# Optimization experiments

Hardware: AMD Instinct MI355X
Metric: run time of the kernel (lower is better)

## Reference

```python
import jax, jax.numpy as jnp
import numpy as np

V, E, H, A, L = 32000, 512, 1024, 1024, 2
B, T, S = 16, 64, 64


def gru_cell(x, h, W_ih, W_hh, b_ih, b_hh):
    # torch GRUCell math: gates ordered (r, z, n)
    gx = x @ W_ih.T + b_ih
    gh = h @ W_hh.T + b_hh
    xr, xz, xn = jnp.split(gx, 3, axis=-1)
    hr, hz, hn = jnp.split(gh, 3, axis=-1)
    r = jax.nn.sigmoid(xr + hr)
    z = jax.nn.sigmoid(xz + hz)
    n = jnp.tanh(xn + r * hn)
    return (1.0 - z) * n + z * h


def setup_inputs() -> dict:
    key = jax.random.key(0)
    ks = jax.random.split(key, 20)
    s = 0.02
    return {
        "tgt": jax.random.randint(ks[0], (B, T), 0, V),
        "hidden": jax.random.normal(ks[1], (L, B, H), jnp.float32) * 0.1,
        "encoder_outputs": jax.random.normal(ks[2], (B, S, H), jnp.float32),
        "emb": jax.random.normal(ks[3], (V, E), jnp.float32) * s,
        "Wq": jax.random.normal(ks[4], (H, A), jnp.float32) * s,
        "Wk": jax.random.normal(ks[5], (H, A), jnp.float32) * s,
        "v_att": jax.random.normal(ks[6], (A,), jnp.float32) * s,
        "W_ih0": jax.random.normal(ks[7], (3 * H, E + H), jnp.float32) * s,
        "W_hh0": jax.random.normal(ks[8], (3 * H, H), jnp.float32) * s,
        "b_ih0": jnp.zeros((3 * H,), jnp.float32),
        "b_hh0": jnp.zeros((3 * H,), jnp.float32),
        "W_ih1": jax.random.normal(ks[9], (3 * H, H), jnp.float32) * s,
        "W_hh1": jax.random.normal(ks[10], (3 * H, H), jnp.float32) * s,
        "b_ih1": jnp.zeros((3 * H,), jnp.float32),
        "b_hh1": jnp.zeros((3 * H,), jnp.float32),
        "W_out": jax.random.normal(ks[11], (V, H), jnp.float32) * s,
        "b_out": jnp.zeros((V,), jnp.float32),
    }


def reference(tgt, hidden, encoder_outputs, emb, Wq, Wk, v_att,
              W_ih0, W_hh0, b_ih0, b_hh0, W_ih1, W_hh1, b_ih1, b_hh1,
              W_out, b_out):
    # Teacher forcing (ratio=1.0), dropout in eval mode (identity).
    keys_proj = jnp.einsum('bsh,ha->bsa', encoder_outputs, Wk)  # precompute W_k K
    emb_tok = emb[tgt]  # [B,T,E]

    def step(carry, x_t):
        h0, h1 = carry  # each [B,H]
        # Bahdanau attention: query = last-layer hidden
        q = jnp.einsum('bh,ha->ba', h1, Wq)
        scores = jnp.einsum('bsa,a->bs', jnp.tanh(q[:, None, :] + keys_proj), v_att)
        attn = jax.nn.softmax(scores, axis=-1)
        ctx = jnp.einsum('bs,bsh->bh', attn, encoder_outputs)
        rnn_in = jnp.concatenate([x_t, ctx], axis=-1)  # [B, E+H]
        h0n = gru_cell(rnn_in, h0, W_ih0, W_hh0, b_ih0, b_hh0)
        h1n = gru_cell(h0n, h1, W_ih1, W_hh1, b_ih1, b_hh1)
        logits = h1n @ W_out.T + b_out  # [B,V]
        return (h0n, h1n), logits

    (_, _), logits = jax.lax.scan(step, (hidden[0], hidden[1]),
                                  jnp.swapaxes(emb_tok, 0, 1))  # xs: [T,B,E]
    return jnp.swapaxes(logits, 0, 1)  # [B,T,V]
```

## Files before the change

kernel.cpp:

```cpp
#include <hip/hip_runtime.h>
#include <hip/hip_bf16.h>
#include <math.h>

typedef __bf16 bf16x8 __attribute__((ext_vector_type(8)));
typedef float  f32x4  __attribute__((ext_vector_type(4)));

__device__ __forceinline__ float sigm(float x){ return 1.0f/(1.0f+expf(-x)); }
__device__ __forceinline__ f32x4 ld4(const float* p){ return *(const f32x4*)p; }
__device__ __forceinline__ void split2(float x, __bf16* h, __bf16* l){
  __bf16 hh = (__bf16)x; *h = hh; *l = (__bf16)(x - (float)hh);
}

__global__ __launch_bounds__(256) void k_transpose(const float* __restrict__ in,
                                                   float* __restrict__ out, int R, int C){
  __shared__ float tile[32][33];
  int c0 = blockIdx.x*32, r0 = blockIdx.y*32;
  int tx = threadIdx.x & 31, ty = threadIdx.x >> 5;
  for(int i=ty;i<32;i+=8) tile[i][tx] = in[(size_t)(r0+i)*C + c0+tx];
  __syncthreads();
  for(int i=ty;i<32;i+=8) out[(size_t)(c0+i)*R + r0+tx] = tile[tx][i];
}

__global__ __launch_bounds__(256) void k_gather(const int* __restrict__ tgt,
                                                const float* __restrict__ emb,
                                                float* __restrict__ emb_tok){
  int m = blockIdx.x;
  int t = m >> 4, b = m & 15;
  int row = tgt[b*64 + t];
  const float* src = emb + (size_t)row*512;
  float* dst = emb_tok + (size_t)m*512;
  for(int e=threadIdx.x;e<512;e+=256) dst[e] = src[e];
}

__global__ __launch_bounds__(256) void k_gemm_s(
    const float* __restrict__ A, int lda,
    const float* __restrict__ Bt, int ldb,
    const float* __restrict__ bias,
    float* __restrict__ C, int N, int K)
{
  __shared__ __align__(16) __bf16 Ash[128][40];
  __shared__ __align__(16) __bf16 Asl[128][40];
  __shared__ __align__(16) __bf16 Bsh[64][40];
  __shared__ __align__(16) __bf16 Bsl[64][40];
  int tid = threadIdx.x;
  int m0 = blockIdx.x*128, n0 = blockIdx.y*64;
  int lane = tid & 63, wave = tid >> 6;
  int wr = wave >> 1, wc = wave & 1;
  int qq = lane >> 4, rr = lane & 15;
  f32x4 acc[4][2] = {};
  int ar = tid >> 1, ak = (tid & 1)*16;
  int br = tid >> 2, bk = (tid & 3)*8;
  for(int k0=0;k0<K;k0+=32){
    const float* ap = A + (size_t)(m0+ar)*lda + k0 + ak;
    f32x4 a0 = ld4(ap), a1 = ld4(ap+4), a2 = ld4(ap+8), a3 = ld4(ap+12);
    const float* bp = Bt + (size_t)(n0+br)*ldb + k0 + bk;
    f32x4 b0 = ld4(bp), b1 = ld4(bp+4);
    __syncthreads();
    #pragma unroll
    for(int e=0;e<4;++e){
      split2(a0[e], &Ash[ar][ak+e],    &Asl[ar][ak+e]);
      split2(a1[e], &Ash[ar][ak+4+e],  &Asl[ar][ak+4+e]);
      split2(a2[e], &Ash[ar][ak+8+e],  &Asl[ar][ak+8+e]);
      split2(a3[e], &Ash[ar][ak+12+e], &Asl[ar][ak+12+e]);
      split2(b0[e], &Bsh[br][bk+e],    &Bsl[br][bk+e]);
      split2(b1[e], &Bsh[br][bk+4+e],  &Bsl[br][bk+4+e]);
    }
    __syncthreads();
    bf16x8 afh[4], afl[4], bfh[2], bfl[2];
    #pragma unroll
    for(int mi=0;mi<4;++mi){
      afh[mi] = *(const bf16x8*)&Ash[wr*64 + mi*16 + rr][qq*8];
      afl[mi] = *(const bf16x8*)&Asl[wr*64 + mi*16 + rr][qq*8];
    }
    #pragma unroll
    for(int ni=0;ni<2;++ni){
      bfh[ni] = *(const bf16x8*)&Bsh[wc*32 + ni*16 + rr][qq*8];
      bfl[ni] = *(const bf16x8*)&Bsl[wc*32 + ni*16 + rr][qq*8];
    }
    #pragma unroll
    for(int mi=0;mi<4;++mi)
      #pragma unroll
      for(int ni=0;ni<2;++ni){
        acc[mi][ni] = __builtin_amdgcn_mfma_f32_16x16x32_bf16(afh[mi], bfh[ni], acc[mi][ni], 0,0,0);
        acc[mi][ni] = __builtin_amdgcn_mfma_f32_16x16x32_bf16(afl[mi], bfh[ni], acc[mi][ni], 0,0,0);
        acc[mi][ni] = __builtin_amdgcn_mfma_f32_16x16x32_bf16(afh[mi], bfl[ni], acc[mi][ni], 0,0,0);
      }
  }
  #pragma unroll
  for(int mi=0;mi<4;++mi)
    #pragma unroll
    for(int ni=0;ni<2;++ni)
      #pragma unroll
      for(int i=0;i<4;++i){
        int m = m0 + wr*64 + mi*16 + qq*4 + i;
        int n = n0 + wc*32 + ni*16 + rr;
        C[(size_t)m*N + n] = acc[mi][ni][i] + (bias? bias[n] : 0.f);
      }
}

__global__ __launch_bounds__(256) void k_pack_w(const float* __restrict__ W,
                                                __bf16* __restrict__ Wp){
  int jt = blockIdx.x, tid = threadIdx.x;
  #pragma unroll
  for(int it=0; it<8; ++it){
    int pos = it*256 + tid;
    int kt = pos>>6, l = pos&63;
    const float* src = W + (size_t)(jt*16 + (l&15))*1024 + kt*32 + (l>>4)*8;
    f32x4 s0 = ld4(src), s1 = ld4(src+4);
    bf16x8 vh, vl;
    #pragma unroll
    for(int e=0;e<4;++e){
      __bf16 h, lo;
      split2(s0[e], &h, &lo); vh[e]   = h; vl[e]   = lo;
      split2(s1[e], &h, &lo); vh[4+e] = h; vl[4+e] = lo;
    }
    __bf16* dst = Wp + ((size_t)(jt*32 + kt))*1024 + l*8;
    *(bf16x8*)dst       = vh;
    *(bf16x8*)(dst+512) = vl;
  }
}

__global__ __launch_bounds__(256) void k_split_h(const float* __restrict__ hidden,
    __bf16* __restrict__ h0h, __bf16* __restrict__ h0l,
    __bf16* __restrict__ h1h, __bf16* __restrict__ h1l){
  int i = blockIdx.x*256 + threadIdx.x;
  float x = hidden[i];
  if(i < 16384) split2(x, &h0h[i], &h0l[i]);
  else { int j = i - 16384; split2(x, &h1h[j], &h1l[j]); }
}

__device__ __forceinline__ void mfma_gemv16(const __bf16* __restrict__ hh,
                                            const __bf16* __restrict__ hl,
                                            const __bf16* __restrict__ Wp, int jt,
                                            float* __restrict__ out, int ldo,
                                            f32x4* red){
  int tid = threadIdx.x, lane = tid & 63, w = tid >> 6;
  const __bf16* Ah = hh + (lane&15)*1024 + (lane>>4)*8;
  const __bf16* Al = hl + (lane&15)*1024 + (lane>>4)*8;
  const __bf16* Bp = Wp + ((size_t)jt*32 + w*8)*1024 + lane*8;
  f32x4 acc = {0.f,0.f,0.f,0.f};
  #pragma unroll
  for(int kk=0;kk<8;++kk){
    int k0 = (w*8 + kk)*32;
    bf16x8 ah = *(const bf16x8*)(Ah + k0);
    bf16x8 al = *(const bf16x8*)(Al + k0);
    bf16x8 bh = *(const bf16x8*)(Bp + kk*1024);
    bf16x8 bl = *(const bf16x8*)(Bp + kk*1024 + 512);
    acc = __builtin_amdgcn_mfma_f32_16x16x32_bf16(ah, bh, acc, 0,0,0);
    acc = __builtin_amdgcn_mfma_f32_16x16x32_bf16(al, bh, acc, 0,0,0);
    acc = __builtin_amdgcn_mfma_f32_16x16x32_bf16(ah, bl, acc, 0,0,0);
  }
  red[w*64 + lane] = acc;
  __syncthreads();
  if(tid < 64){
    f32x4 s = red[tid] + red[64+tid] + red[128+tid] + red[192+tid];
    int j = jt*16 + (tid & 15);
    #pragma unroll
    for(int i=0;i<4;++i) out[(size_t)((tid>>4)*4 + i)*ldo + j] = s[i];
  }
}

__global__ __launch_bounds__(256) void k_boot(const __bf16* __restrict__ hh,
                                              const __bf16* __restrict__ hl,
                                              const __bf16* __restrict__ Wp,
                                              float* __restrict__ gh0){
  __shared__ f32x4 red[256];
  mfma_gemv16(hh, hl, Wp, blockIdx.x, gh0, 3072, red);
}

__global__ __launch_bounds__(256) void k_step1(const __bf16* __restrict__ h1h,
                                               const __bf16* __restrict__ h1l,
                                               const __bf16* __restrict__ Whh1p,
                                               const __bf16* __restrict__ Wqp,
                                               float* __restrict__ gh1,
                                               float* __restrict__ q){
  __shared__ f32x4 red[256];
  int blk = blockIdx.x;
  if(blk < 192) mfma_gemv16(h1h, h1l, Whh1p, blk,     gh1, 3072, red);
  else          mfma_gemv16(h1h, h1l, Wqp,   blk-192, q,   1024, red);
}

__global__ __launch_bounds__(512) void k_step2(const float* __restrict__ q,
                                               const float* __restrict__ kp,
                                               const float* __restrict__ v_att,
                                               float* __restrict__ escore){
  int pair = blockIdx.x*8 + (threadIdx.x >> 6);
  int b = pair >> 6;
  int lane = threadIdx.x & 63;
  const float* qp  = q  + b*1024 + lane*16;
  const float* kpp = kp + (size_t)pair*1024 + lane*16;
  const float* vp  = v_att + lane*16;
  float acc = 0.f;
  #pragma unroll
  for(int i=0;i<4;++i){
    f32x4 qv = ld4(qp+i*4), kv = ld4(kpp+i*4), vv = ld4(vp+i*4);
    #pragma unroll
    for(int e=0;e<4;++e) acc += vv[e]*tanhf(qv[e]+kv[e]);
  }
  #pragma unroll
  for(int o=1;o<64;o<<=1) acc += __shfl_xor(acc, o);
  if(lane==0) escore[pair] = expf(acc);
}

__global__ __launch_bounds__(512) void k_step3(int t,
    const float* __restrict__ escore, const float* __restrict__ EW,
    const float* __restrict__ GX0x, const float* __restrict__ gh0,
    const float* __restrict__ b_hh0,
    const float* __restrict__ h0_in, float* __restrict__ h0_out,
    __bf16* __restrict__ h0h, __bf16* __restrict__ h0l)
{
  __shared__ float part[8][4][16][3];
  __shared__ float dred[4][16];
  __shared__ float sden[4];
  int blk = blockIdx.x, tid = threadIdx.x;
  int jt = blk >> 2, bq = blk & 3;
  int lane = tid & 63, w = tid >> 6;
  int bl = lane >> 4, jl = lane & 15;
  int b = bq*4 + bl;
  int col = jt*16 + jl;
  float a0=0.f, a1=0.f, a2=0.f;
  const float* ep  = escore + b*64 + w*8;
  const float* ewp = EW + ((size_t)(b*64 + w*8))*3072 + col;
  #pragma unroll
  for(int si=0; si<8; ++si){
    float e = ep[si];
    const float* r = ewp + (size_t)si*3072;
    a0 += e*r[0]; a1 += e*r[1024]; a2 += e*r[2048];
  }
  part[w][bl][jl][0]=a0; part[w][bl][jl][1]=a1; part[w][bl][jl][2]=a2;
  if(tid < 64){
    int bb = tid >> 4, si = tid & 15;
    const float* e2 = escore + (bq*4 + bb)*64;
    dred[bb][si] = e2[si] + e2[si+16] + e2[si+32] + e2[si+48];
  }
  __syncthreads();
  if(tid < 4){
    float d = 0.f;
    #pragma unroll
    for(int i=0;i<16;++i) d += dred[tid][i];
    sden[tid] = d;
  }
  __syncthreads();
  if(tid < 64){
    float xr=0.f, xz=0.f, xn=0.f;
    #pragma unroll
    for(int k=0;k<8;++k){ xr+=part[k][bl][jl][0]; xz+=part[k][bl][jl][1]; xn+=part[k][bl][jl][2]; }
    float inv = 1.0f / sden[bl];
    int j = col;
    const float* gx = GX0x + ((size_t)t*16 + b)*3072 + j;
    const float* g0 = gh0 + (size_t)b*3072 + j;
    float r = sigm(xr*inv + gx[0]    + g0[0]    + b_hh0[j]);
    float z = sigm(xz*inv + gx[1024] + g0[1024] + b_hh0[1024+j]);
    float n = tanhf(xn*inv + gx[2048] + r*(g0[2048] + b_hh0[2048+j]));
    float hnew = (1.f-z)*n + z*h0_in[b*1024 + j];
    h0_out[b*1024 + j] = hnew;
    split2(hnew, &h0h[b*1024 + j], &h0l[b*1024 + j]);
  }
}

__global__ __launch_bounds__(256) void k_step4(int t,
    const __bf16* __restrict__ h0h, const __bf16* __restrict__ h0l,
    const __bf16* __restrict__ Wih1p, const __bf16* __restrict__ Whh0p,
    const float* __restrict__ b_ih1, const float* __restrict__ b_hh1,
    const float* __restrict__ gh1,
    const float* __restrict__ h1_in, float* __restrict__ h1_out,
    __bf16* __restrict__ h1h, __bf16* __restrict__ h1l,
    __bf16* __restrict__ Hb, float* __restrict__ gh0)
{
  __shared__ f32x4 red[256];
  __shared__ float xg[3][16][16];
  int blk = blockIdx.x, tid = threadIdx.x;
  if(blk >= 64){
    mfma_gemv16(h0h, h0l, Whh0p, blk-64, gh0, 3072, red);
    return;
  }
  int lane = tid & 63, w = tid >> 6;
  const __bf16* Ah = h0h + (lane&15)*1024 + (lane>>4)*8;
  const __bf16* Al = h0l + (lane&15)*1024 + (lane>>4)*8;
  #pragma unroll
  for(int g=0; g<3; ++g){
    int jt = g*64 + blk;
    const __bf16* Bp = Wih1p + ((size_t)jt*32 + w*8)*1024 + lane*8;
    f32x4 acc = {0.f,0.f,0.f,0.f};
    #pragma unroll
    for(int kk=0;kk<8;++kk){
      int k0 = (w*8 + kk)*32;
      bf16x8 ah = *(const bf16x8*)(Ah + k0);
      bf16x8 al = *(const bf16x8*)(Al + k0);
      bf16x8 bh = *(const bf16x8*)(Bp + kk*1024);
      bf16x8 bl = *(const bf16x8*)(Bp + kk*1024 + 512);
      acc = __builtin_amdgcn_mfma_f32_16x16x32_bf16(ah, bh, acc, 0,0,0);
      acc = __builtin_amdgcn_mfma_f32_16x16x32_bf16(al, bh, acc, 0,0,0);
      acc = __builtin_amdgcn_mfma_f32_16x16x32_bf16(ah, bl, acc, 0,0,0);
    }
    if(g) __syncthreads();
    red[w*64 + lane] = acc;
    __syncthreads();
    if(tid < 64){
      f32x4 s = red[tid] + red[64+tid] + red[128+tid] + red[192+tid];
      #pragma unroll
      for(int i=0;i<4;++i) xg[g][(tid>>4)*4 + i][tid&15] = s[i];
    }
  }
  __syncthreads();
  int b = tid >> 4, jl = tid & 15, j = blk*16 + jl;
  float xr = xg[0][b][jl] + b_ih1[j];
  float xz = xg[1][b][jl] + b_ih1[1024+j];
  float xn = xg[2][b][jl] + b_ih1[2048+j];
  const float* g1 = gh1 + (size_t)b*3072 + j;
  float r = sigm(xr + g1[0]    + b_hh1[j]);
  float z = sigm(xz + g1[1024] + b_hh1[1024+j]);
  float n = tanhf(xn + r*(g1[2048] + b_hh1[2048+j]));
  float hnew = (1.f-z)*n + z*h1_in[b*1024 + j];
  h1_out[b*1024 + j] = hnew;
  split2(hnew, &h1h[b*1024 + j], &h1l[b*1024 + j]);
  Hb[((size_t)t*16 + b)*1024 + j] = (__bf16)hnew;
}

__global__ __launch_bounds__(512) void k_logits(
    const __bf16* __restrict__ Hb, const float* __restrict__ Wout,
    const float* __restrict__ b_out, float* __restrict__ out)
{
  int c = blockIdx.x & 7, j = blockIdx.x >> 3;
  int x = j & 3, y = (j >> 2)*8 + c;
  if(y >= 250) return;
  int tm0 = x*256, tn0 = y*128;
  __shared__ __align__(16) __bf16 As[256][40];
  __shared__ __align__(16) __bf16 Bs[128][40];
  int tid = threadIdx.x;
  int lane = tid & 63, wave = tid >> 6;
  int wr = wave >> 1, wc = wave & 1;
  int qq = lane >> 4, rr = lane & 15;
  f32x4 acc[4][4] = {};
  int ar = tid >> 2, ak = (tid & 3) * 8;
  for(int k0=0;k0<1024;k0+=32){
    bf16x8 a0v = *(const bf16x8*)(Hb + (size_t)(tm0+ar)*1024     + k0 + ak);
    bf16x8 a1v = *(const bf16x8*)(Hb + (size_t)(tm0+ar+128)*1024 + k0 + ak);
    const float* bp = Wout + (size_t)(tn0+ar)*1024 + k0 + ak;
    f32x4 f0 = ld4(bp), f1 = ld4(bp+4);
    __syncthreads();
    *(bf16x8*)&As[ar][ak]     = a0v;
    *(bf16x8*)&As[ar+128][ak] = a1v;
    bf16x8 bv;
    #pragma unroll
    for(int i=0;i<4;++i){ bv[i]=(__bf16)f0[i]; bv[4+i]=(__bf16)f1[i]; }
    *(bf16x8*)&Bs[ar][ak] = bv;
    __syncthreads();
    bf16x8 af[4], bfr[4];
    #pragma unroll
    for(int mi=0;mi<4;++mi) af[mi]  = *(const bf16x8*)&As[wr*64 + mi*16 + rr][qq*8];
    #pragma unroll
    for(int ni=0;ni<4;++ni) bfr[ni] = *(const bf16x8*)&Bs[wc*64 + ni*16 + rr][qq*8];
    #pragma unroll
    for(int mi=0;mi<4;++mi)
      #pragma unroll
      for(int ni=0;ni<4;++ni)
        acc[mi][ni] = __builtin_amdgcn_mfma_f32_16x16x32_bf16(af[mi], bfr[ni], acc[mi][ni], 0,0,0);
  }
  #pragma unroll
  for(int mi=0;mi<4;++mi)
    #pragma unroll
    for(int ni=0;ni<4;++ni)
      #pragma unroll
      for(int i=0;i<4;++i){
        int m = tm0 + wr*64 + mi*16 + qq*4 + i;
        int v = tn0 + wc*64 + ni*16 + rr;
        int bb = m & 15, tt = m >> 4;
        out[((size_t)bb*64 + tt)*32000 + v] = acc[mi][ni][i] + b_out[v];
      }
}

extern "C" void kernel_launch(void* const* d_in, const int* in_sizes, int n_in,
                              void* d_out, int out_size, void* d_ws, size_t ws_size,
                              hipStream_t stream){
  const int*   tgt    = (const int*)d_in[0];
  const float* hidden = (const float*)d_in[1];
  const float* enc    = (const float*)d_in[2];
  const float* emb    = (const float*)d_in[3];
  const float* Wq     = (const float*)d_in[4];
  const float* Wk     = (const float*)d_in[5];
  const float* v_att  = (const float*)d_in[6];
  const float* W_ih0  = (const float*)d_in[7];
  const float* W_hh0  = (const float*)d_in[8];
  const float* b_ih0  = (const float*)d_in[9];
  const float* b_hh0  = (const float*)d_in[10];
  const float* W_ih1  = (const float*)d_in[11];
  const float* W_hh1  = (const float*)d_in[12];
  const float* b_ih1  = (const float*)d_in[13];
  const float* b_hh1  = (const float*)d_in[14];
  const float* W_out  = (const float*)d_in[15];
  const float* b_out  = (const float*)d_in[16];
  float* out = (float*)d_out;

  float* ws = (float*)d_ws;
  size_t off = 0;
  auto alloc = [&](size_t n){ float* p = ws + off; off += n; return p; };
  float*  kp     = alloc((size_t)1024*1024);
  float*  GX0x   = alloc((size_t)1024*3072);
  float*  EW     = alloc((size_t)1024*3072);
  __bf16* Whh0p  = (__bf16*)alloc((size_t)3072*1024);
  __bf16* Whh1p  = (__bf16*)alloc((size_t)3072*1024);
  __bf16* Wih1p  = (__bf16*)alloc((size_t)3072*1024);
  __bf16* Wqp    = (__bf16*)alloc((size_t)1024*1024);
  float*  gh0    = alloc((size_t)16*3072);
  float*  gh1    = alloc((size_t)16*3072);
  float*  q      = alloc((size_t)16*1024);
  float*  escore = alloc((size_t)16*64);
  float*  h0A    = alloc((size_t)16*1024);
  float*  h0B    = alloc((size_t)16*1024);
  float*  h1A    = alloc((size_t)16*1024);
  float*  h1B    = alloc((size_t)16*1024);
  __bf16* h0sh   = (__bf16*)alloc((size_t)8192);
  __bf16* h0sl   = (__bf16*)alloc((size_t)8192);
  __bf16* h1sh   = (__bf16*)alloc((size_t)8192);
  __bf16* h1sl   = (__bf16*)alloc((size_t)8192);
  __bf16* Hb     = (__bf16*)alloc((size_t)512*1024);
  float*  REGION = alloc((size_t)1572864);
  float*  emb_tok = REGION;
  float*  WT      = REGION + 524288;
  (void)ws_size; (void)in_sizes; (void)n_in; (void)out_size;

  k_gather<<<1024,256,0,stream>>>(tgt, emb, emb_tok);
  k_transpose<<<dim3(32,32),256,0,stream>>>(Wk, WT, 1024, 1024);
  k_gemm_s<<<dim3(8,16),256,0,stream>>>(enc,1024, WT,1024, nullptr, kp, 1024, 1024);
  k_gemm_s<<<dim3(8,48),256,0,stream>>>(emb_tok,512, W_ih0,1536, b_ih0, GX0x, 3072, 512);
  k_gemm_s<<<dim3(8,48),256,0,stream>>>(enc,1024, W_ih0+512,1536, nullptr, EW, 3072, 1024);
  k_transpose<<<dim3(32,32),256,0,stream>>>(Wq, WT, 1024, 1024);
  k_pack_w<<<64,256,0,stream>>>(WT, Wqp);
  k_pack_w<<<192,256,0,stream>>>(W_hh0, Whh0p);
  k_pack_w<<<192,256,0,stream>>>(W_hh1, Whh1p);
  k_pack_w<<<192,256,0,stream>>>(W_ih1, Wih1p);
  k_split_h<<<128,256,0,stream>>>(hidden, h0sh, h0sl, h1sh, h1sl);
  k_boot<<<192,256,0,stream>>>(h0sh, h0sl, Whh0p, gh0);

  for(int t=0;t<64;++t){
    const float* h0i = (t==0)? hidden            : ((t&1)? h0A : h0B);
    float*       h0o = (t&1)? h0B : h0A;
    const float* h1i = (t==0)? hidden + 16*1024  : ((t&1)? h1A : h1B);
    float*       h1o = (t&1)? h1B : h1A;
    k_step1<<<256,256,0,stream>>>(h1sh, h1sl, Whh1p, Wqp, gh1, q);
    k_step2<<<128,512,0,stream>>>(q, kp, v_att, escore);
    k_step3<<<256,512,0,stream>>>(t, escore, EW, GX0x, gh0, b_hh0, h0i, h0o, h0sh, h0sl);
    k_step4<<<256,256,0,stream>>>(t, h0sh, h0sl, Wih1p, Whh0p, b_ih1, b_hh1, gh1,
                                  h1i, h1o, h1sh, h1sl, Hb, gh0);
  }

  k_logits<<<1024,512,0,stream>>>(Hb, W_out, b_out, out);
}
```

Before: 2.093 ms.

## Fuse attention scoring into query GEMV kernel and pre-convert W_out to bf16

Combines the Wq projection with partial attention score computation per 16-wide slice, moving softmax reduction into the GRU0 update kernel, so each timestep uses three launches instead of four. GEMV blocks are widened to 8 waves with shorter K loops per wave. Wq is packed directly from its original layout instead of via a transpose, and W_out is converted to bf16 once before the logits GEMM to halve its reads there. This adds an extra conversion pass and workspace aliasing that must not overlap live data.

Result: slower. 2.166 ms (+3.5%).

```diff
diff --git a/kernel.cpp b/kernel.cpp
--- a/kernel.cpp
+++ b/kernel.cpp
@@ -4,6 +4,8 @@
 
 typedef __bf16 bf16x8 __attribute__((ext_vector_type(8)));
 typedef float  f32x4  __attribute__((ext_vector_type(4)));
+
+#define MFMA16 __builtin_amdgcn_mfma_f32_16x16x32_bf16
 
 __device__ __forceinline__ float sigm(float x){ return 1.0f/(1.0f+expf(-x)); }
 __device__ __forceinline__ f32x4 ld4(const float* p){ return *(const f32x4*)p; }
@@ -81,9 +83,9 @@
     for(int mi=0;mi<4;++mi)
       #pragma unroll
       for(int ni=0;ni<2;++ni){
-        acc[mi][ni] = __builtin_amdgcn_mfma_f32_16x16x32_bf16(afh[mi], bfh[ni], acc[mi][ni], 0,0,0);
-        acc[mi][ni] = __builtin_amdgcn_mfma_f32_16x16x32_bf16(afl[mi], bfh[ni], acc[mi][ni], 0,0,0);
-        acc[mi][ni] = __builtin_amdgcn_mfma_f32_16x16x32_bf16(afh[mi], bfl[ni], acc[mi][ni], 0,0,0);
+        acc[mi][ni] = MFMA16(afh[mi], bfh[ni], acc[mi][ni], 0,0,0);
+        acc[mi][ni] = MFMA16(afl[mi], bfh[ni], acc[mi][ni], 0,0,0);
+        acc[mi][ni] = MFMA16(afh[mi], bfl[ni], acc[mi][ni], 0,0,0);
       }
   }
   #pragma unroll
@@ -120,6 +122,28 @@
   }
 }
 
+__global__ __launch_bounds__(256) void k_pack_wT(const float* __restrict__ W, int ldw,
+                                                 __bf16* __restrict__ Wp){
+  int jt = blockIdx.x, tid = threadIdx.x;
+  #pragma unroll
+  for(int it=0; it<8; ++it){
+    int pos = it*256 + tid;
+    int kt = pos>>6, l = pos&63;
+    int j = jt*16 + (l&15);
+    int kbase = kt*32 + (l>>4)*8;
+    bf16x8 vh, vl;
+    #pragma unroll
+    for(int e=0;e<8;++e){
+      float x = W[(size_t)(kbase+e)*ldw + j];
+      __bf16 h = (__bf16)x;
+      vh[e] = h; vl[e] = (__bf16)(x - (float)h);
+    }
+    __bf16* dst = Wp + ((size_t)(jt*32 + kt))*1024 + l*8;
+    *(bf16x8*)dst       = vh;
+    *(bf16x8*)(dst+512) = vl;
+  }
+}
+
 __global__ __launch_bounds__(256) void k_split_h(const float* __restrict__ hidden,
     __bf16* __restrict__ h0h, __bf16* __restrict__ h0l,
     __bf16* __restrict__ h1h, __bf16* __restrict__ h1l){
@@ -129,136 +153,181 @@
   else { int j = i - 16384; split2(x, &h1h[j], &h1l[j]); }
 }
 
-__device__ __forceinline__ void mfma_gemv16(const __bf16* __restrict__ hh,
-                                            const __bf16* __restrict__ hl,
-                                            const __bf16* __restrict__ Wp, int jt,
-                                            float* __restrict__ out, int ldo,
-                                            f32x4* red){
+__global__ __launch_bounds__(256) void k_cvt16(const float* __restrict__ in,
+                                               __bf16* __restrict__ out){
+  int i = blockIdx.x*256 + threadIdx.x;
+  const float* p = in + (size_t)i*8;
+  f32x4 f0 = ld4(p), f1 = ld4(p+4);
+  bf16x8 v;
+  #pragma unroll
+  for(int e=0;e<4;++e){ v[e] = (__bf16)f0[e]; v[4+e] = (__bf16)f1[e]; }
+  *(bf16x8*)(out + (size_t)i*8) = v;
+}
+
+__device__ __forceinline__ void gemv_w8(const __bf16* __restrict__ hh,
+                                        const __bf16* __restrict__ hl,
+                                        const __bf16* __restrict__ Wp, int jt,
+                                        float* __restrict__ out, int ldo,
+                                        f32x4* red){
   int tid = threadIdx.x, lane = tid & 63, w = tid >> 6;
   const __bf16* Ah = hh + (lane&15)*1024 + (lane>>4)*8;
   const __bf16* Al = hl + (lane&15)*1024 + (lane>>4)*8;
-  const __bf16* Bp = Wp + ((size_t)jt*32 + w*8)*1024 + lane*8;
+  const __bf16* Bp = Wp + ((size_t)jt*32 + w*4)*1024 + lane*8;
   f32x4 acc = {0.f,0.f,0.f,0.f};
   #pragma unroll
-  for(int kk=0;kk<8;++kk){
-    int k0 = (w*8 + kk)*32;
+  for(int kk=0;kk<4;++kk){
+    int k0 = (w*4 + kk)*32;
     bf16x8 ah = *(const bf16x8*)(Ah + k0);
     bf16x8 al = *(const bf16x8*)(Al + k0);
     bf16x8 bh = *(const bf16x8*)(Bp + kk*1024);
     bf16x8 bl = *(const bf16x8*)(Bp + kk*1024 + 512);
-    acc = __builtin_amdgcn_mfma_f32_16x16x32_bf16(ah, bh, acc, 0,0,0);
-    acc = __builtin_amdgcn_mfma_f32_16x16x32_bf16(al, bh, acc, 0,0,0);
-    acc = __builtin_amdgcn_mfma_f32_16x16x32_bf16(ah, bl, acc, 0,0,0);
+    acc = MFMA16(ah, bh, acc, 0,0,0);
+    acc = MFMA16(al, bh, acc, 0,0,0);
+    acc = MFMA16(ah, bl, acc, 0,0,0);
   }
   red[w*64 + lane] = acc;
   __syncthreads();
   if(tid < 64){
-    f32x4 s = red[tid] + red[64+tid] + red[128+tid] + red[192+tid];
+    f32x4 s = red[tid];
+    #pragma unroll
+    for(int k=1;k<8;++k) s += red[k*64 + tid];
     int j = jt*16 + (tid & 15);
     #pragma unroll
     for(int i=0;i<4;++i) out[(size_t)((tid>>4)*4 + i)*ldo + j] = s[i];
   }
 }
 
-__global__ __launch_bounds__(256) void k_boot(const __bf16* __restrict__ hh,
+__global__ __launch_bounds__(512) void k_boot(const __bf16* __restrict__ hh,
                                               const __bf16* __restrict__ hl,
                                               const __bf16* __restrict__ Wp,
                                               float* __restrict__ gh0){
-  __shared__ f32x4 red[256];
-  mfma_gemv16(hh, hl, Wp, blockIdx.x, gh0, 3072, red);
-}
-
-__global__ __launch_bounds__(256) void k_step1(const __bf16* __restrict__ h1h,
-                                               const __bf16* __restrict__ h1l,
-                                               const __bf16* __restrict__ Whh1p,
-                                               const __bf16* __restrict__ Wqp,
-                                               float* __restrict__ gh1,
-                                               float* __restrict__ q){
-  __shared__ f32x4 red[256];
-  int blk = blockIdx.x;
-  if(blk < 192) mfma_gemv16(h1h, h1l, Whh1p, blk,     gh1, 3072, red);
-  else          mfma_gemv16(h1h, h1l, Wqp,   blk-192, q,   1024, red);
-}
-
-__global__ __launch_bounds__(512) void k_step2(const float* __restrict__ q,
-                                               const float* __restrict__ kp,
-                                               const float* __restrict__ v_att,
-                                               float* __restrict__ escore){
-  int pair = blockIdx.x*8 + (threadIdx.x >> 6);
-  int b = pair >> 6;
-  int lane = threadIdx.x & 63;
-  const float* qp  = q  + b*1024 + lane*16;
-  const float* kpp = kp + (size_t)pair*1024 + lane*16;
-  const float* vp  = v_att + lane*16;
-  float acc = 0.f;
-  #pragma unroll
-  for(int i=0;i<4;++i){
-    f32x4 qv = ld4(qp+i*4), kv = ld4(kpp+i*4), vv = ld4(vp+i*4);
-    #pragma unroll
-    for(int e=0;e<4;++e) acc += vv[e]*tanhf(qv[e]+kv[e]);
-  }
-  #pragma unroll
-  for(int o=1;o<64;o<<=1) acc += __shfl_xor(acc, o);
-  if(lane==0) escore[pair] = expf(acc);
-}
-
-__global__ __launch_bounds__(512) void k_step3(int t,
-    const float* __restrict__ escore, const float* __restrict__ EW,
+  __shared__ f32x4 red[512];
+  gemv_w8(hh, hl, Wp, blockIdx.x, gh0, 3072, red);
+}
+
+__global__ __launch_bounds__(512) void k_SA(
+    const __bf16* __restrict__ h1h, const __bf16* __restrict__ h1l,
+    const __bf16* __restrict__ Whh1p, const __bf16* __restrict__ Wqp,
+    const float* __restrict__ kp, const float* __restrict__ v_att,
+    float* __restrict__ gh1, float* __restrict__ parts)
+{
+  __shared__ f32x4 red[512];
+  __shared__ float qs[16][16];
+  int blk = blockIdx.x, tid = threadIdx.x;
+  if(blk < 192){ gemv_w8(h1h, h1l, Whh1p, blk, gh1, 3072, red); return; }
+  int slice = blk - 192;
+  {
+    int lane = tid & 63, w = tid >> 6;
+    const __bf16* Ah = h1h + (lane&15)*1024 + (lane>>4)*8;
+    const __bf16* Al = h1l + (lane&15)*1024 + (lane>>4)*8;
+    const __bf16* Bp = Wqp + ((size_t)slice*32 + w*4)*1024 + lane*8;
+    f32x4 acc = {0.f,0.f,0.f,0.f};
+    #pragma unroll
+    for(int kk=0;kk<4;++kk){
+      int k0 = (w*4 + kk)*32;
+      bf16x8 ah = *(const bf16x8*)(Ah + k0);
+      bf16x8 al = *(const bf16x8*)(Al + k0);
+      bf16x8 bh = *(const bf16x8*)(Bp + kk*1024);
+      bf16x8 bl = *(const bf16x8*)(Bp + kk*1024 + 512);
+      acc = MFMA16(ah, bh, acc, 0,0,0);
+      acc = MFMA16(al, bh, acc, 0,0,0);
+      acc = MFMA16(ah, bl, acc, 0,0,0);
+    }
+    red[w*64 + lane] = acc;
+    __syncthreads();
+    if(tid < 64){
+      f32x4 s = red[tid];
+      #pragma unroll
+      for(int k=1;k<8;++k) s += red[k*64 + tid];
+      #pragma unroll
+      for(int i=0;i<4;++i) qs[(tid>>4)*4 + i][tid&15] = s[i];
+    }
+    __syncthreads();
+  }
+  const float* vp = v_att + slice*16;
+  f32x4 v0 = ld4(vp), v1 = ld4(vp+4), v2 = ld4(vp+8), v3 = ld4(vp+12);
+  #pragma unroll
+  for(int r=0;r<2;++r){
+    int pair = r*512 + tid;
+    int b = pair >> 6;
+    const float* kpr = kp + (size_t)pair*1024 + slice*16;
+    f32x4 c0 = ld4(kpr), c1 = ld4(kpr+4), c2 = ld4(kpr+8), c3 = ld4(kpr+12);
+    float acc = 0.f;
+    #pragma unroll
+    for(int e=0;e<4;++e){
+      acc += v0[e]*tanhf(qs[b][e]     + c0[e]);
+      acc += v1[e]*tanhf(qs[b][4+e]   + c1[e]);
+      acc += v2[e]*tanhf(qs[b][8+e]   + c2[e]);
+      acc += v3[e]*tanhf(qs[b][12+e]  + c3[e]);
+    }
+    parts[(size_t)slice*1024 + pair] = acc;
+  }
+}
+
+__global__ __launch_bounds__(512) void k_SB(int t,
+    const float* __restrict__ parts, const float* __restrict__ EW,
     const float* __restrict__ GX0x, const float* __restrict__ gh0,
     const float* __restrict__ b_hh0,
     const float* __restrict__ h0_in, float* __restrict__ h0_out,
     __bf16* __restrict__ h0h, __bf16* __restrict__ h0l)
 {
+  __shared__ float ssum[256][2];
+  __shared__ float sc[4][64];
+  __shared__ float sden[4];
   __shared__ float part[8][4][16][3];
-  __shared__ float dred[4][16];
-  __shared__ float sden[4];
   int blk = blockIdx.x, tid = threadIdx.x;
   int jt = blk >> 2, bq = blk & 3;
+  {
+    int p = tid >> 1, hf = tid & 1;
+    int pair = bq*256 + p;
+    const float* pp = parts + (size_t)(hf*32)*1024 + pair;
+    float s = 0.f;
+    #pragma unroll
+    for(int k=0;k<32;++k) s += pp[(size_t)k*1024];
+    ssum[p][hf] = s;
+  }
+  __syncthreads();
+  if(tid < 256) sc[tid>>6][tid&63] = expf(ssum[tid][0] + ssum[tid][1]);
+  __syncthreads();
+  if(tid < 4){
+    float d = 0.f;
+    #pragma unroll
+    for(int s2=0;s2<64;++s2) d += sc[tid][s2];
+    sden[tid] = d;
+  }
+  __syncthreads();
   int lane = tid & 63, w = tid >> 6;
   int bl = lane >> 4, jl = lane & 15;
-  int b = bq*4 + bl;
-  int col = jt*16 + jl;
+  int b = bq*4 + bl, col = jt*16 + jl;
   float a0=0.f, a1=0.f, a2=0.f;
-  const float* ep  = escore + b*64 + w*8;
   const float* ewp = EW + ((size_t)(b*64 + w*8))*3072 + col;
   #pragma unroll
   for(int si=0; si<8; ++si){
-    float e = ep[si];
-    const float* r = ewp + (size_t)si*3072;
-    a0 += e*r[0]; a1 += e*r[1024]; a2 += e*r[2048];
+    float e = sc[bl][w*8 + si];
+    const float* r2 = ewp + (size_t)si*3072;
+    a0 += e*r2[0]; a1 += e*r2[1024]; a2 += e*r2[2048];
   }
   part[w][bl][jl][0]=a0; part[w][bl][jl][1]=a1; part[w][bl][jl][2]=a2;
+  __syncthreads();
   if(tid < 64){
-    int bb = tid >> 4, si = tid & 15;
-    const float* e2 = escore + (bq*4 + bb)*64;
-    dred[bb][si] = e2[si] + e2[si+16] + e2[si+32] + e2[si+48];
-  }
-  __syncthreads();
-  if(tid < 4){
-    float d = 0.f;
-    #pragma unroll
-    for(int i=0;i<16;++i) d += dred[tid][i];
-    sden[tid] = d;
-  }
-  __syncthreads();
-  if(tid < 64){
+    int bl2 = tid >> 4, jl2 = tid & 15;
+    int b2 = bq*4 + bl2, j = jt*16 + jl2;
     float xr=0.f, xz=0.f, xn=0.f;
     #pragma unroll
-    for(int k=0;k<8;++k){ xr+=part[k][bl][jl][0]; xz+=part[k][bl][jl][1]; xn+=part[k][bl][jl][2]; }
-    float inv = 1.0f / sden[bl];
-    int j = col;
-    const float* gx = GX0x + ((size_t)t*16 + b)*3072 + j;
-    const float* g0 = gh0 + (size_t)b*3072 + j;
+    for(int k=0;k<8;++k){ xr+=part[k][bl2][jl2][0]; xz+=part[k][bl2][jl2][1]; xn+=part[k][bl2][jl2][2]; }
+    float inv = 1.0f / sden[bl2];
+    const float* gx = GX0x + ((size_t)t*16 + b2)*3072 + j;
+    const float* g0 = gh0 + (size_t)b2*3072 + j;
     float r = sigm(xr*inv + gx[0]    + g0[0]    + b_hh0[j]);
     float z = sigm(xz*inv + gx[1024] + g0[1024] + b_hh0[1024+j]);
     float n = tanhf(xn*inv + gx[2048] + r*(g0[2048] + b_hh0[2048+j]));
-    float hnew = (1.f-z)*n + z*h0_in[b*1024 + j];
-    h0_out[b*1024 + j] = hnew;
-    split2(hnew, &h0h[b*1024 + j], &h0l[b*1024 + j]);
-  }
-}
-
-__global__ __launch_bounds__(256) void k_step4(int t,
+    float hnew = (1.f-z)*n + z*h0_in[b2*1024 + j];
+    h0_out[b2*1024 + j] = hnew;
+    split2(hnew, &h0h[b2*1024 + j], &h0l[b2*1024 + j]);
+  }
+}
+
+__global__ __launch_bounds__(512) void k_SC(int t,
     const __bf16* __restrict__ h0h, const __bf16* __restrict__ h0l,
     const __bf16* __restrict__ Wih1p, const __bf16* __restrict__ Whh0p,
     const float* __restrict__ b_ih1, const float* __restrict__ b_hh1,
@@ -267,58 +336,58 @@
     __bf16* __restrict__ h1h, __bf16* __restrict__ h1l,
     __bf16* __restrict__ Hb, float* __restrict__ gh0)
 {
-  __shared__ f32x4 red[256];
+  __shared__ f32x4 red[1536];
   __shared__ float xg[3][16][16];
   int blk = blockIdx.x, tid = threadIdx.x;
-  if(blk >= 64){
-    mfma_gemv16(h0h, h0l, Whh0p, blk-64, gh0, 3072, red);
-    return;
-  }
+  if(blk >= 64){ gemv_w8(h0h, h0l, Whh0p, blk-64, gh0, 3072, red); return; }
   int lane = tid & 63, w = tid >> 6;
   const __bf16* Ah = h0h + (lane&15)*1024 + (lane>>4)*8;
   const __bf16* Al = h0l + (lane&15)*1024 + (lane>>4)*8;
   #pragma unroll
   for(int g=0; g<3; ++g){
-    int jt = g*64 + blk;
-    const __bf16* Bp = Wih1p + ((size_t)jt*32 + w*8)*1024 + lane*8;
+    const __bf16* Bp = Wih1p + ((size_t)(g*64 + blk)*32 + w*4)*1024 + lane*8;
     f32x4 acc = {0.f,0.f,0.f,0.f};
     #pragma unroll
-    for(int kk=0;kk<8;++kk){
-      int k0 = (w*8 + kk)*32;
+    for(int kk=0;kk<4;++kk){
+      int k0 = (w*4 + kk)*32;
       bf16x8 ah = *(const bf16x8*)(Ah + k0);
       bf16x8 al = *(const bf16x8*)(Al + k0);
       bf16x8 bh = *(const bf16x8*)(Bp + kk*1024);
       bf16x8 bl = *(const bf16x8*)(Bp + kk*1024 + 512);
-      acc = __builtin_amdgcn_mfma_f32_16x16x32_bf16(ah, bh, acc, 0,0,0);
-      acc = __builtin_amdgcn_mfma_f32_16x16x32_bf16(al, bh, acc, 0,0,0);
-      acc = __builtin_amdgcn_mfma_f32_16x16x32_bf16(ah, bl, acc, 0,0,0);
-    }
-    if(g) __syncthreads();
-    red[w*64 + lane] = acc;
-    __syncthreads();
-    if(tid < 64){
-      f32x4 s = red[tid] + red[64+tid] + red[128+tid] + red[192+tid];
-      #pragma unroll
-      for(int i=0;i<4;++i) xg[g][(tid>>4)*4 + i][tid&15] = s[i];
-    }
-  }
-  __syncthreads();
-  int b = tid >> 4, jl = tid & 15, j = blk*16 + jl;
-  float xr = xg[0][b][jl] + b_ih1[j];
-  float xz = xg[1][b][jl] + b_ih1[1024+j];
-  float xn = xg[2][b][jl] + b_ih1[2048+j];
-  const float* g1 = gh1 + (size_t)b*3072 + j;
-  float r = sigm(xr + g1[0]    + b_hh1[j]);
-  float z = sigm(xz + g1[1024] + b_hh1[1024+j]);
-  float n = tanhf(xn + r*(g1[2048] + b_hh1[2048+j]));
-  float hnew = (1.f-z)*n + z*h1_in[b*1024 + j];
-  h1_out[b*1024 + j] = hnew;
-  split2(hnew, &h1h[b*1024 + j], &h1l[b*1024 + j]);
-  Hb[((size_t)t*16 + b)*1024 + j] = (__bf16)hnew;
+      acc = MFMA16(ah, bh, acc, 0,0,0);
+      acc = MFMA16(al, bh, acc, 0,0,0);
+      acc = MFMA16(ah, bl, acc, 0,0,0);
+    }
+    red[g*512 + w*64 + lane] = acc;
+  }
+  __syncthreads();
+  if(tid < 192){
+    int g = tid >> 6, tt = tid & 63;
+    f32x4 s = red[g*512 + tt];
+    #pragma unroll
+    for(int k=1;k<8;++k) s += red[g*512 + k*64 + tt];
+    #pragma unroll
+    for(int i=0;i<4;++i) xg[g][(tt>>4)*4 + i][tt&15] = s[i];
+  }
+  __syncthreads();
+  if(tid < 256){
+    int b = tid >> 4, jl = tid & 15, j = blk*16 + jl;
+    float xr = xg[0][b][jl] + b_ih1[j];
+    float xz = xg[1][b][jl] + b_ih1[1024+j];
+    float xn = xg[2][b][jl] + b_ih1[2048+j];
+    const float* g1 = gh1 + (size_t)b*3072 + j;
+    float r = sigm(xr + g1[0]    + b_hh1[j]);
+    float z = sigm(xz + g1[1024] + b_hh1[1024+j]);
+    float n = tanhf(xn + r*(g1[2048] + b_hh1[2048+j]));
+    float hnew = (1.f-z)*n + z*h1_in[b*1024 + j];
+    h1_out[b*1024 + j] = hnew;
+    split2(hnew, &h1h[b*1024 + j], &h1l[b*1024 + j]);
+    Hb[((size_t)t*16 + b)*1024 + j] = (__bf16)hnew;
+  }
 }
 
 __global__ __launch_bounds__(512) void k_logits(
-    const __bf16* __restrict__ Hb, const float* __restrict__ Wout,
+    const __bf16* __restrict__ Hb, const __bf16* __restrict__ Wb,
     const float* __restrict__ b_out, float* __restrict__ out)
 {
   int c = blockIdx.x & 7, j = blockIdx.x >> 3;
@@ -336,15 +405,11 @@
   for(int k0=0;k0<1024;k0+=32){
     bf16x8 a0v = *(const bf16x8*)(Hb + (size_t)(tm0+ar)*1024     + k0 + ak);
     bf16x8 a1v = *(const bf16x8*)(Hb + (size_t)(tm0+ar+128)*1024 + k0 + ak);
-    const float* bp = Wout + (size_t)(tn0+ar)*1024 + k0 + ak;
-    f32x4 f0 = ld4(bp), f1 = ld4(bp+4);
+    bf16x8 bv  = *(const bf16x8*)(Wb + (size_t)(tn0+ar)*1024     + k0 + ak);
     __syncthreads();
     *(bf16x8*)&As[ar][ak]     = a0v;
     *(bf16x8*)&As[ar+128][ak] = a1v;
-    bf16x8 bv;
-    #pragma unroll
-    for(int i=0;i<4;++i){ bv[i]=(__bf16)f0[i]; bv[4+i]=(__bf16)f1[i]; }
-    *(bf16x8*)&Bs[ar][ak] = bv;
+    *(bf16x8*)&Bs[ar][ak]     = bv;
     __syncthreads();
     bf16x8 af[4], bfr[4];
     #pragma unroll
@@ -355,7 +420,7 @@
     for(int mi=0;mi<4;++mi)
       #pragma unroll
       for(int ni=0;ni<4;++ni)
-        acc[mi][ni] = __builtin_amdgcn_mfma_f32_16x16x32_bf16(af[mi], bfr[ni], acc[mi][ni], 0,0,0);
+        acc[mi][ni] = MFMA16(af[mi], bfr[ni], acc[mi][ni], 0,0,0);
   }
   #pragma unroll
   for(int mi=0;mi<4;++mi)
@@ -404,8 +469,7 @@
   __bf16* Wqp    = (__bf16*)alloc((size_t)1024*1024);
   float*  gh0    = alloc((size_t)16*3072);
   float*  gh1    = alloc((size_t)16*3072);
-  float*  q      = alloc((size_t)16*1024);
-  float*  escore = alloc((size_t)16*64);
+  float*  parts  = alloc((size_t)64*1024);
   float*  h0A    = alloc((size_t)16*1024);
   float*  h0B    = alloc((size_t)16*1024);
   float*  h1A    = alloc((size_t)16*1024);
@@ -414,10 +478,11 @@
   __bf16* h0sl   = (__bf16*)alloc((size_t)8192);
   __bf16* h1sh   = (__bf16*)alloc((size_t)8192);
   __bf16* h1sl   = (__bf16*)alloc((size_t)8192);
-  __bf16* Hb     = (__bf16*)alloc((size_t)512*1024);
-  float*  REGION = alloc((size_t)1572864);
-  float*  emb_tok = REGION;
-  float*  WT      = REGION + 524288;
+  float*  Hb_f   = alloc((size_t)512*1024);
+  __bf16* Hb     = (__bf16*)Hb_f;
+  float*  emb_tok = Hb_f;
+  float*  WT      = EW;
+  __bf16* Woutb   = (__bf16*)ws;
   (void)ws_size; (void)in_sizes; (void)n_in; (void)out_size;
 
   k_gather<<<1024,256,0,stream>>>(tgt, emb, emb_tok);
@@ -425,25 +490,24 @@
   k_gemm_s<<<dim3(8,16),256,0,stream>>>(enc,1024, WT,1024, nullptr, kp, 1024, 1024);
   k_gemm_s<<<dim3(8,48),256,0,stream>>>(emb_tok,512, W_ih0,1536, b_ih0, GX0x, 3072, 512);
   k_gemm_s<<<dim3(8,48),256,0,stream>>>(enc,1024, W_ih0+512,1536, nullptr, EW, 3072, 1024);
-  k_transpose<<<dim3(32,32),256,0,stream>>>(Wq, WT, 1024, 1024);
-  k_pack_w<<<64,256,0,stream>>>(WT, Wqp);
+  k_pack_wT<<<64,256,0,stream>>>(Wq, 1024, Wqp);
   k_pack_w<<<192,256,0,stream>>>(W_hh0, Whh0p);
   k_pack_w<<<192,256,0,stream>>>(W_hh1, Whh1p);
   k_pack_w<<<192,256,0,stream>>>(W_ih1, Wih1p);
   k_split_h<<<128,256,0,stream>>>(hidden, h0sh, h0sl, h1sh, h1sl);
-  k_boot<<<192,256,0,stream>>>(h0sh, h0sl, Whh0p, gh0);
+  k_boot<<<192,512,0,stream>>>(h0sh, h0sl, Whh0p, gh0);
 
   for(int t=0;t<64;++t){
     const float* h0i = (t==0)? hidden            : ((t&1)? h0A : h0B);
     float*       h0o = (t&1)? h0B : h0A;
     const float* h1i = (t==0)? hidden + 16*1024  : ((t&1)? h1A : h1B);
     float*       h1o = (t&1)? h1B : h1A;
-    k_step1<<<256,256,0,stream>>>(h1sh, h1sl, Whh1p, Wqp, gh1, q);
-    k_step2<<<128,512,0,stream>>>(q, kp, v_att, escore);
-    k_step3<<<256,512,0,stream>>>(t, escore, EW, GX0x, gh0, b_hh0, h0i, h0o, h0sh, h0sl);
-    k_step4<<<256,256,0,stream>>>(t, h0sh, h0sl, Wih1p, Whh0p, b_ih1, b_hh1, gh1,
-                                  h1i, h1o, h1sh, h1sl, Hb, gh0);
-  }
-
-  k_logits<<<1024,512,0,stream>>>(Hb, W_out, b_out, out);
-}
+    k_SA<<<256,512,0,stream>>>(h1sh, h1sl, Whh1p, Wqp, kp, v_att, gh1, parts);
+    k_SB<<<256,512,0,stream>>>(t, parts, EW, GX0x, gh0, b_hh0, h0i, h0o, h0sh, h0sl);
+    k_SC<<<256,512,0,stream>>>(t, h0sh, h0sl, Wih1p, Whh0p, b_ih1, b_hh1, gh1,
+                               h1i, h1o, h1sh, h1sl, Hb, gh0);
+  }
+
+  k_cvt16<<<16000,256,0,stream>>>(W_out, Woutb);
+  k_logits<<<1024,512,0,stream>>>(Hb, Woutb, b_out, out);
+}
```
